# Performance work log

Hardware: AMD Instinct MI355X
Metric: run time of the kernel (lower is better)

The kernel has to match this reference:

```python
import jax, jax.numpy as jnp
import numpy as np

N = 50000   # nodes
E = 640000  # edges
H = 128     # input/hidden dim
C = 40      # classes
L = 2       # gnn layers


def _layernorm(h, g, b, eps=1e-5):
    mu = jnp.mean(h, axis=-1, keepdims=True)
    var = jnp.mean((h - mu) ** 2, axis=-1, keepdims=True)
    return (h - mu) * jax.lax.rsqrt(var + eps) * g + b


def setup_inputs() -> dict:
    key = jax.random.key(0)
    ks = jax.random.split(key, 20)
    s = 0.02
    inp = {
        "x": jax.random.normal(ks[0], (N, H), dtype=jnp.float32),
        "edge_index": jax.random.randint(ks[1], (2, E), 0, N, dtype=jnp.int64),
        # input projection MLP (Linear->ReLU->Dropout(eval)->Linear)
        "proj_w1": jax.random.normal(ks[2], (H, H), dtype=jnp.float32) * s,
        "proj_b1": jnp.zeros((H,), jnp.float32),
        "proj_w2": jax.random.normal(ks[3], (H, H), dtype=jnp.float32) * s,
        "proj_b2": jnp.zeros((H,), jnp.float32),
        "in_norm_g": jnp.ones((H,), jnp.float32),
        "in_norm_b": jnp.zeros((H,), jnp.float32),
        # stacked SAGEConv params: lin_l (on mean-aggregated neighbors, with bias),
        # lin_r (root weight, no bias) -- PyG SAGEConv defaults
        "sage_wl": jax.random.normal(ks[4], (L, H, H), dtype=jnp.float32) * s,
        "sage_bl": jnp.zeros((L, H), jnp.float32),
        "sage_wr": jax.random.normal(ks[5], (L, H, H), dtype=jnp.float32) * s,
        "ln_g": jnp.ones((L, H), jnp.float32),
        "ln_b": jnp.zeros((L, H), jnp.float32),
        # classifier MLP
        "cls_w1": jax.random.normal(ks[6], (H, H), dtype=jnp.float32) * s,
        "cls_b1": jnp.zeros((H,), jnp.float32),
        "cls_w2": jax.random.normal(ks[7], (H, C), dtype=jnp.float32) * s,
        "cls_b2": jnp.zeros((C,), jnp.float32),
    }
    return inp


def reference(x, edge_index, proj_w1, proj_b1, proj_w2, proj_b2,
              in_norm_g, in_norm_b, sage_wl, sage_bl, sage_wr,
              ln_g, ln_b, cls_w1, cls_b1, cls_w2, cls_b2):
    src = edge_index[0]  # message sources x_j
    dst = edge_index[1]  # aggregation targets
    # in-degree counts for mean aggregation (isolated nodes -> 0 output)
    cnt = jax.ops.segment_sum(jnp.ones((E,), jnp.float32), dst, num_segments=N)
    inv_cnt = jnp.where(cnt > 0, 1.0 / jnp.maximum(cnt, 1.0), 0.0)[:, None]

    # input projection + norm (dropout is identity in eval mode)
    h = jax.nn.relu(x @ proj_w1 + proj_b1) @ proj_w2 + proj_b2
    h = _layernorm(h, in_norm_g, in_norm_b)

    for l in range(L):
        msg_sum = jax.ops.segment_sum(h[src], dst, num_segments=N)  # [N,H]
        agg = msg_sum * inv_cnt  # mean aggregation
        h_next = agg @ sage_wl[l] + sage_bl[l] + h @ sage_wr[l]  # SAGEConv
        h_next = jax.nn.relu(h_next)
        h = _layernorm(h + h_next, ln_g[l], ln_b[l])  # residual + LayerNorm

    logits = jax.nn.relu(h @ cls_w1 + cls_b1) @ cls_w2 + cls_b2
    return (logits, h)
```

## Files before the change

### kernel.cpp

```cpp
#include <hip/hip_runtime.h>


namespace {

constexpr int NN = 50000;
constexpr int EE = 640000;
constexpr int HH = 128;
constexpr int CC = 40;
constexpr int SCAN_NB = (NN + 255) / 256;
constexpr int MG = (NN + 127) / 128;
constexpr int DEGB = (EE + 255) / 256;
constexpr int WPB = (5 * 16384 + CC * 128 + 255) / 256;

typedef unsigned short u16;
typedef __attribute__((ext_vector_type(8))) short s16x8;
typedef __attribute__((ext_vector_type(8))) unsigned short u16x8;
typedef __attribute__((ext_vector_type(4))) float f32x4;
typedef __attribute__((ext_vector_type(2))) float f32x2;

__device__ __forceinline__ float b2f(u16 h) {
  unsigned int u = ((unsigned int)h) << 16;
  return __builtin_bit_cast(float, u);
}
__device__ __forceinline__ u16 f2b(float f) {
  unsigned int u = __builtin_bit_cast(unsigned int, f);
  u += 0x7FFFu + ((u >> 16) & 1u);
  return (u16)(u >> 16);
}

__device__ __forceinline__ uint2 pack_fp8(const float* v) {
  int w0 = 0, w1 = 0;
  w0 = __builtin_amdgcn_cvt_pk_fp8_f32(v[0], v[1], w0, false);
  w0 = __builtin_amdgcn_cvt_pk_fp8_f32(v[2], v[3], w0, true);
  w1 = __builtin_amdgcn_cvt_pk_fp8_f32(v[4], v[5], w1, false);
  w1 = __builtin_amdgcn_cvt_pk_fp8_f32(v[6], v[7], w1, true);
  return make_uint2((unsigned)w0, (unsigned)w1);
}
__device__ __forceinline__ void acc_fp8(float* a, uint2 p) {
  const f32x2 f0 = __builtin_amdgcn_cvt_pk_f32_fp8((int)p.x, false);
  const f32x2 f1 = __builtin_amdgcn_cvt_pk_f32_fp8((int)p.x, true);
  const f32x2 f2 = __builtin_amdgcn_cvt_pk_f32_fp8((int)p.y, false);
  const f32x2 f3 = __builtin_amdgcn_cvt_pk_f32_fp8((int)p.y, true);
  a[0] += f0.x; a[1] += f0.y; a[2] += f1.x; a[3] += f1.y;
  a[4] += f2.x; a[5] += f2.y; a[6] += f3.x; a[7] += f3.y;
}

__device__ __forceinline__ s16x8 ldsw(const u16* base, int n, int k0) {
  return *reinterpret_cast<const s16x8*>(base + n * 128 + (((k0 ^ n) & 15) << 3));
}
__device__ __forceinline__ void stsw(u16* base, int r, int c, u16 v) {
  base[r * 128 + ((((c >> 3) ^ r) & 15) << 3) + (c & 7)] = v;
}
template <int NGRAN>
__device__ __forceinline__ void stage(const u16* __restrict__ src, u16* dst, int tid) {
#pragma unroll
  for (int i = 0; i < (NGRAN + 255) / 256; ++i) {
    const int gi = i * 256 + tid;
    if ((NGRAN & 255) == 0 || gi < NGRAN) {
      const int n = gi >> 4, k0 = gi & 15;
      const u16x8 v = *reinterpret_cast<const u16x8*>(src + gi * 8);
      *reinterpret_cast<u16x8*>(dst + n * 128 + (((k0 ^ n) & 15) << 3)) = v;
    }
  }
}

__global__ void k_pre(const float* __restrict__ pw1, const float* __restrict__ pw2,
                      u16* __restrict__ wt, int* __restrict__ cnt) {
  int flat = blockIdx.x * 256 + threadIdx.x;
  const int TWO = 2 * 16384;
  if (flat < TWO) {
    int id = flat >> 14;
    int off = flat & 16383;
    int n = off >> 7, k = off & 127;
    const float* s = id == 0 ? pw1 : pw2;
    wt[(size_t)id * 16384 + n * 128 + k] = f2b(s[k * 128 + n]);
  } else {
    int i = flat - TWO;
    if (i < NN) cnt[i] = 0;
  }
}

__global__ void k_scan_block(const int* __restrict__ cnt, int* __restrict__ rowptr,
                             int* __restrict__ bsum, float* __restrict__ inv) {
  __shared__ int s[256];
  const int t = threadIdx.x;
  const int i = blockIdx.x * 256 + t;
  const int v = i < NN ? cnt[i] : 0;
  s[t] = v;
  __syncthreads();
  for (int off = 1; off < 256; off <<= 1) {
    int add = t >= off ? s[t - off] : 0;
    __syncthreads();
    s[t] += add;
    __syncthreads();
  }
  if (i < NN) {
    rowptr[i] = s[t] - v;
    inv[i] = v > 0 ? 1.0f / (float)v : 0.0f;
  }
  if (t == 255) bsum[blockIdx.x] = s[255];
}

__global__ void k_scan_add(int* __restrict__ rowptr, const int* __restrict__ bsum) {
  __shared__ int s[256];
  const int t = threadIdx.x;
  const int v = t < SCAN_NB ? bsum[t] : 0;
  s[t] = v;
  __syncthreads();
  for (int off = 1; off < 256; off <<= 1) {
    int add = t >= off ? s[t - off] : 0;
    __syncthreads();
    s[t] += add;
    __syncthreads();
  }
  const int boff = blockIdx.x == 0 ? 0 : s[blockIdx.x - 1];
  const int i = blockIdx.x * 256 + t;
  if (i < NN) rowptr[i] += boff;
  if (i == 0) rowptr[NN] = EE;
}

__global__ void k_fill(const int* __restrict__ ei, const int* __restrict__ rowptr,
                       const int* __restrict__ rank, int* __restrict__ col) {
  int e = blockIdx.x * 256 + threadIdx.x;
  if (e >= EE) return;
  const int d = ei[EE + e];
  col[rowptr[d] + rank[e]] = ei[e];
}

__global__ __launch_bounds__(256) void k_gather8(
    const unsigned char* __restrict__ h8, const int* __restrict__ rowptr,
    const int* __restrict__ col, const float* __restrict__ inv,
    u16* __restrict__ agg) {
  const int tid = threadIdx.x;
  const int node = blockIdx.x * 16 + (tid >> 4);
  if (node >= NN) return;
  const int ln = tid & 15;
  const int cl = ln * 8;
  const int start = rowptr[node];
  const int end = rowptr[node + 1];
  float a[8] = {0.f, 0.f, 0.f, 0.f, 0.f, 0.f, 0.f, 0.f};
  int i = start;
  for (; i + 8 <= end; i += 8) {
    const uint2 p0 = *reinterpret_cast<const uint2*>(&h8[(size_t)col[i] * 128 + cl]);
    const uint2 p1 = *reinterpret_cast<const uint2*>(&h8[(size_t)col[i + 1] * 128 + cl]);
    const uint2 p2 = *reinterpret_cast<const uint2*>(&h8[(size_t)col[i + 2] * 128 + cl]);
    const uint2 p3 = *reinterpret_cast<const uint2*>(&h8[(size_t)col[i + 3] * 128 + cl]);
    const uint2 p4 = *reinterpret_cast<const uint2*>(&h8[(size_t)col[i + 4] * 128 + cl]);
    const uint2 p5 = *reinterpret_cast<const uint2*>(&h8[(size_t)col[i + 5] * 128 + cl]);
    const uint2 p6 = *reinterpret_cast<const uint2*>(&h8[(size_t)col[i + 6] * 128 + cl]);
    const uint2 p7 = *reinterpret_cast<const uint2*>(&h8[(size_t)col[i + 7] * 128 + cl]);
    acc_fp8(a, p0); acc_fp8(a, p1); acc_fp8(a, p2); acc_fp8(a, p3);
    acc_fp8(a, p4); acc_fp8(a, p5); acc_fp8(a, p6); acc_fp8(a, p7);
  }
  if (i + 4 <= end) {
    const uint2 p0 = *reinterpret_cast<const uint2*>(&h8[(size_t)col[i] * 128 + cl]);
    const uint2 p1 = *reinterpret_cast<const uint2*>(&h8[(size_t)col[i + 1] * 128 + cl]);
    const uint2 p2 = *reinterpret_cast<const uint2*>(&h8[(size_t)col[i + 2] * 128 + cl]);
    const uint2 p3 = *reinterpret_cast<const uint2*>(&h8[(size_t)col[i + 3] * 128 + cl]);
    acc_fp8(a, p0); acc_fp8(a, p1); acc_fp8(a, p2); acc_fp8(a, p3);
    i += 4;
  }
  for (; i < end; ++i) {
    const uint2 p0 = *reinterpret_cast<const uint2*>(&h8[(size_t)col[i] * 128 + cl]);
    acc_fp8(a, p0);
  }
  const float sc = inv[node];
#pragma unroll
  for (int k = 0; k < 8; ++k)
    agg[(size_t)node * 128 + k * 16 + ln] = f2b(a[k] * sc);
}

__global__ __launch_bounds__(256) void k_mlp_deg(
    const float* __restrict__ x, const u16* __restrict__ WT1,
    const float* __restrict__ pb1, const u16* __restrict__ WT2,
    const float* __restrict__ pb2, const float* __restrict__ lg,
    const float* __restrict__ lb, u16* __restrict__ hb,
    unsigned char* __restrict__ h8,
    const int* __restrict__ ei, int* __restrict__ cnt, int* __restrict__ rank,
    const float* __restrict__ swl, const float* __restrict__ swr,
    const float* __restrict__ cw1, const float* __restrict__ cw2,
    u16* __restrict__ wt) {
  __shared__ u16 lds[32768];
  if (blockIdx.x >= MG) {
    const int rb = blockIdx.x - MG;
    if (rb < DEGB) {
      const int e = rb * 256 + threadIdx.x;
      if (e < EE) rank[e] = atomicAdd(&cnt[ei[EE + e]], 1);
    } else {
      const int flat = (rb - DEGB) * 256 + threadIdx.x;
      const int FIVE = 5 * 16384;
      if (flat < FIVE) {
        int id = flat >> 14;
        int off = flat & 16383;
        int n = off >> 7, k = off & 127;
        const float* s;
        switch (id) {
          case 0: s = swl; break;
          case 1: s = swl + 16384; break;
          case 2: s = swr; break;
          case 3: s = swr + 16384; break;
          default: s = cw1; break;
        }
        wt[(size_t)(id + 2) * 16384 + n * 128 + k] = f2b(s[k * 128 + n]);
      } else {
        int off = flat - FIVE;
        if (off < CC * 128) {
          int n = off >> 7, k = off & 127;
          wt[(size_t)7 * 16384 + n * 128 + k] = f2b(cw2[k * CC + n]);
        }
      }
    }
    return;
  }
  u16* wreg = lds;
  u16* t1r = lds + 16384;
  const int tid = threadIdx.x;
  const int wv = tid >> 6, ln = tid & 63;
  const int lrow = ln & 15, kg = ln >> 4;
  const int tbase = blockIdx.x * 128 + wv * 32;
  const int lb0 = wv * 32;
  const int ar0 = min(tbase + lrow, NN - 1);
  const int ar1 = min(tbase + 16 + lrow, NN - 1);

  stage<2048>(WT1, wreg, tid);
  __syncthreads();

  f32x4 acc0[8], acc1[8];
#pragma unroll
  for (int cf = 0; cf < 8; ++cf) {
    acc0[cf] = (f32x4){0.f, 0.f, 0.f, 0.f};
    acc1[cf] = (f32x4){0.f, 0.f, 0.f, 0.f};
  }
#pragma unroll
  for (int ks = 0; ks < 4; ++ks) {
    const float4* p0 = reinterpret_cast<const float4*>(x + (size_t)ar0 * 128 + ks * 32 + kg * 8);
    const float4* p1 = reinterpret_cast<const float4*>(x + (size_t)ar1 * 128 + ks * 32 + kg * 8);
    float4 x0 = p0[0], x1 = p0[1], y0 = p1[0], y1 = p1[1];
    s16x8 a0, a1;
    a0[0] = (short)f2b(x0.x); a0[1] = (short)f2b(x0.y); a0[2] = (short)f2b(x0.z); a0[3] = (short)f2b(x0.w);
    a0[4] = (short)f2b(x1.x); a0[5] = (short)f2b(x1.y); a0[6] = (short)f2b(x1.z); a0[7] = (short)f2b(x1.w);
    a1[0] = (short)f2b(y0.x); a1[1] = (short)f2b(y0.y); a1[2] = (short)f2b(y0.z); a1[3] = (short)f2b(y0.w);
    a1[4] = (short)f2b(y1.x); a1[5] = (short)f2b(y1.y); a1[6] = (short)f2b(y1.z); a1[7] = (short)f2b(y1.w);
#pragma unroll
    for (int cf = 0; cf < 8; ++cf) {
      const s16x8 bf = ldsw(wreg, cf * 16 + lrow, ks * 4 + kg);
      acc0[cf] = __builtin_amdgcn_mfma_f32_16x16x32_bf16(a0, bf, acc0[cf], 0, 0, 0);
      acc1[cf] = __builtin_amdgcn_mfma_f32_16x16x32_bf16(a1, bf, acc1[cf], 0, 0, 0);
    }
  }
  {
    float bb[8];
#pragma unroll
    for (int cf = 0; cf < 8; ++cf) bb[cf] = pb1[cf * 16 + lrow];
#pragma unroll
    for (int t = 0; t < 2; ++t)
#pragma unroll
      for (int j = 0; j < 4; ++j) {
        const int lr = lb0 + t * 16 + kg * 4 + j;
#pragma unroll
        for (int cf = 0; cf < 8; ++cf)
          stsw(t1r, lr, cf * 16 + lrow, f2b(fmaxf((t ? acc1[cf][j] : acc0[cf][j]) + bb[cf], 0.0f)));
      }
  }
  __syncthreads();
  stage<2048>(WT2, wreg, tid);
  __syncthreads();

  f32x4 c0[8], c1[8];
#pragma unroll
  for (int cf = 0; cf < 8; ++cf) {
    c0[cf] = (f32x4){0.f, 0.f, 0.f, 0.f};
    c1[cf] = (f32x4){0.f, 0.f, 0.f, 0.f};
  }
#pragma unroll
  for (int ks = 0; ks < 4; ++ks) {
    const s16x8 a0 = ldsw(t1r, lb0 + lrow, ks * 4 + kg);
    const s16x8 a1 = ldsw(t1r, lb0 + 16 + lrow, ks * 4 + kg);
#pragma unroll
    for (int cf = 0; cf < 8; ++cf) {
      const s16x8 bf = ldsw(wreg, cf * 16 + lrow, ks * 4 + kg);
      c0[cf] = __builtin_amdgcn_mfma_f32_16x16x32_bf16(a0, bf, c0[cf], 0, 0, 0);
      c1[cf] = __builtin_amdgcn_mfma_f32_16x16x32_bf16(a1, bf, c1[cf], 0, 0, 0);
    }
  }

  float bb[8], gm[8], gb[8];
#pragma unroll
  for (int cf = 0; cf < 8; ++cf) {
    const int c = cf * 16 + lrow;
    bb[cf] = pb2[c];
    gm[cf] = lg[c];
    gb[cf] = lb[c];
  }
#pragma unroll
  for (int t = 0; t < 2; ++t)
#pragma unroll
    for (int j = 0; j < 4; ++j) {
      const int r = tbase + t * 16 + kg * 4 + j;
      float v[8];
#pragma unroll
      for (int cf = 0; cf < 8; ++cf) v[cf] = (t ? c1[cf][j] : c0[cf][j]) + bb[cf];
      float s = 0.f;
#pragma unroll
      for (int cf = 0; cf < 8; ++cf) s += v[cf];
      s += __shfl_xor(s, 1); s += __shfl_xor(s, 2);
      s += __shfl_xor(s, 4); s += __shfl_xor(s, 8);
      const float mu = s * (1.0f / 128);
      float q = 0.f;
#pragma unroll
      for (int cf = 0; cf < 8; ++cf) { const float d = v[cf] - mu; q += d * d; }
      q += __shfl_xor(q, 1); q += __shfl_xor(q, 2);
      q += __shfl_xor(q, 4); q += __shfl_xor(q, 8);
      const float istd = rsqrtf(q * (1.0f / 128) + 1e-5f);
      if (r < NN) {
        float ov[8];
#pragma unroll
        for (int cf = 0; cf < 8; ++cf) {
          ov[cf] = (v[cf] - mu) * istd * gm[cf] + gb[cf];
          hb[(size_t)r * 128 + cf * 16 + lrow] = f2b(ov[cf]);
        }
        *reinterpret_cast<uint2*>(&h8[(size_t)r * 128 + lrow * 8]) = pack_fp8(ov);
      }
    }
}

__global__ __launch_bounds__(256) void k_sage0(
    const u16* __restrict__ agg, const u16* __restrict__ hb,
    const u16* __restrict__ WTl, const u16* __restrict__ WTr,
    const float* __restrict__ bl, const float* __restrict__ lg,
    const float* __restrict__ lb, u16* __restrict__ hb_out,
    unsigned char* __restrict__ h8) {
  __shared__ u16 lds[32768];
  u16* wl = lds;
  u16* wr = lds + 16384;
  const int tid = threadIdx.x;
  const int wv = tid >> 6, ln = tid & 63;
  const int lrow = ln & 15, kg = ln >> 4;
  const int tbase = blockIdx.x * 128 + wv * 32;
  const int ar0 = min(tbase + lrow, NN - 1);
  const int ar1 = min(tbase + 16 + lrow, NN - 1);

  stage<2048>(WTl, wl, tid);
  stage<2048>(WTr, wr, tid);
  __syncthreads();

  f32x4 acc0[8], acc1[8];
#pragma unroll
  for (int cf = 0; cf < 8; ++cf) {
    acc0[cf] = (f32x4){0.f, 0.f, 0.f, 0.f};
    acc1[cf] = (f32x4){0.f, 0.f, 0.f, 0.f};
  }
#pragma unroll
  for (int ks = 0; ks < 4; ++ks) {
    const s16x8 g0 = *reinterpret_cast<const s16x8*>(agg + (size_t)ar0 * 128 + ks * 32 + kg * 8);
    const s16x8 g1 = *reinterpret_cast<const s16x8*>(agg + (size_t)ar1 * 128 + ks * 32 + kg * 8);
    const s16x8 h0 = *reinterpret_cast<const s16x8*>(hb + (size_t)ar0 * 128 + ks * 32 + kg * 8);
    const s16x8 h1 = *reinterpret_cast<const s16x8*>(hb + (size_t)ar1 * 128 + ks * 32 + kg * 8);
#pragma unroll
    for (int cf = 0; cf < 8; ++cf) {
      const s16x8 bwl = ldsw(wl, cf * 16 + lrow, ks * 4 + kg);
      const s16x8 bwr = ldsw(wr, cf * 16 + lrow, ks * 4 + kg);
      acc0[cf] = __builtin_amdgcn_mfma_f32_16x16x32_bf16(g0, bwl, acc0[cf], 0, 0, 0);
      acc0[cf] = __builtin_amdgcn_mfma_f32_16x16x32_bf16(h0, bwr, acc0[cf], 0, 0, 0);
      acc1[cf] = __builtin_amdgcn_mfma_f32_16x16x32_bf16(g1, bwl, acc1[cf], 0, 0, 0);
      acc1[cf] = __builtin_amdgcn_mfma_f32_16x16x32_bf16(h1, bwr, acc1[cf], 0, 0, 0);
    }
  }

  float bb[8], gm[8], gb[8];
#pragma unroll
  for (int cf = 0; cf < 8; ++cf) {
    const int c = cf * 16 + lrow;
    bb[cf] = bl[c];
    gm[cf] = lg[c];
    gb[cf] = lb[c];
  }
#pragma unroll
  for (int t = 0; t < 2; ++t)
#pragma unroll
    for (int j = 0; j < 4; ++j) {
      const int r = tbase + t * 16 + kg * 4 + j;
      const int rs = r < NN ? r : NN - 1;
      float v[8];
#pragma unroll
      for (int cf = 0; cf < 8; ++cf) {
        const int c = cf * 16 + lrow;
        v[cf] = b2f(hb[(size_t)rs * 128 + c]) +
                fmaxf((t ? acc1[cf][j] : acc0[cf][j]) + bb[cf], 0.0f);
      }
      float s = 0.f;
#pragma unroll
      for (int cf = 0; cf < 8; ++cf) s += v[cf];
      s += __shfl_xor(s, 1); s += __shfl_xor(s, 2);
      s += __shfl_xor(s, 4); s += __shfl_xor(s, 8);
      const float mu = s * (1.0f / 128);
      float q = 0.f;
#pragma unroll
      for (int cf = 0; cf < 8; ++cf) { const float d = v[cf] - mu; q += d * d; }
      q += __shfl_xor(q, 1); q += __shfl_xor(q, 2);
      q += __shfl_xor(q, 4); q += __shfl_xor(q, 8);
      const float istd = rsqrtf(q * (1.0f / 128) + 1e-5f);
      if (r < NN) {
        float ov[8];
#pragma unroll
        for (int cf = 0; cf < 8; ++cf) {
          ov[cf] = (v[cf] - mu) * istd * gm[cf] + gb[cf];
          hb_out[(size_t)r * 128 + cf * 16 + lrow] = f2b(ov[cf]);
        }
        *reinterpret_cast<uint2*>(&h8[(size_t)r * 128 + lrow * 8]) = pack_fp8(ov);
      }
    }
}

__global__ __launch_bounds__(256) void k_sage_cls(
    const u16* __restrict__ agg, const u16* __restrict__ hb,
    const u16* __restrict__ WTl, const u16* __restrict__ WTr,
    const float* __restrict__ bl, const float* __restrict__ lg,
    const float* __restrict__ lb,
    const u16* __restrict__ Wc1, const float* __restrict__ cb1,
    const u16* __restrict__ Wc2, const float* __restrict__ cb2,
    float* __restrict__ out_h, float* __restrict__ logits) {
  __shared__ u16 lds[37888];
  u16* wl = lds;
  u16* wr = lds + 16384;
  u16* w2 = lds + 32768;
  const int tid = threadIdx.x;
  const int wv = tid >> 6, ln = tid & 63;
  const int lrow = ln & 15, kg = ln >> 4;
  const int tbase = blockIdx.x * 128 + wv * 32;
  const int lb0 = wv * 32;
  const int ar0 = min(tbase + lrow, NN - 1);
  const int ar1 = min(tbase + 16 + lrow, NN - 1);

  stage<2048>(WTl, wl, tid);
  stage<2048>(WTr, wr, tid);
  stage<640>(Wc2, w2, tid);
  __syncthreads();

  f32x4 acc0[8], acc1[8];
#pragma unroll
  for (int cf = 0; cf < 8; ++cf) {
    acc0[cf] = (f32x4){0.f, 0.f, 0.f, 0.f};
    acc1[cf] = (f32x4){0.f, 0.f, 0.f, 0.f};
  }
#pragma unroll
  for (int ks = 0; ks < 4; ++ks) {
    const s16x8 g0 = *reinterpret_cast<const s16x8*>(agg + (size_t)ar0 * 128 + ks * 32 + kg * 8);
    const s16x8 g1 = *reinterpret_cast<const s16x8*>(agg + (size_t)ar1 * 128 + ks * 32 + kg * 8);
    const s16x8 h0 = *reinterpret_cast<const s16x8*>(hb + (size_t)ar0 * 128 + ks * 32 + kg * 8);
    const s16x8 h1 = *reinterpret_cast<const s16x8*>(hb + (size_t)ar1 * 128 + ks * 32 + kg * 8);
#pragma unroll
    for (int cf = 0; cf < 8; ++cf) {
      const s16x8 bwl = ldsw(wl, cf * 16 + lrow, ks * 4 + kg);
      const s16x8 bwr = ldsw(wr, cf * 16 + lrow, ks * 4 + kg);
      acc0[cf] = __builtin_amdgcn_mfma_f32_16x16x32_bf16(g0, bwl, acc0[cf], 0, 0, 0);
      acc0[cf] = __builtin_amdgcn_mfma_f32_16x16x32_bf16(h0, bwr, acc0[cf], 0, 0, 0);
      acc1[cf] = __builtin_amdgcn_mfma_f32_16x16x32_bf16(g1, bwl, acc1[cf], 0, 0, 0);
      acc1[cf] = __builtin_amdgcn_mfma_f32_16x16x32_bf16(h1, bwr, acc1[cf], 0, 0, 0);
    }
  }
  __syncthreads();

  {
    float bb[8], gm[8], gb[8];
#pragma unroll
    for (int cf = 0; cf < 8; ++cf) {
      const int c = cf * 16 + lrow;
      bb[cf] = bl[c];
      gm[cf] = lg[c];
      gb[cf] = lb[c];
    }
#pragma unroll
    for (int t = 0; t < 2; ++t)
#pragma unroll
      for (int j = 0; j < 4; ++j) {
        const int r = tbase + t * 16 + kg * 4 + j;
        const int rs = r < NN ? r : NN - 1;
        const int lr = lb0 + t * 16 + kg * 4 + j;
        float v[8];
#pragma unroll
        for (int cf = 0; cf < 8; ++cf) {
          const int c = cf * 16 + lrow;
          v[cf] = b2f(hb[(size_t)rs * 128 + c]) +
                  fmaxf((t ? acc1[cf][j] : acc0[cf][j]) + bb[cf], 0.0f);
        }
        float s = 0.f;
#pragma unroll
        for (int cf = 0; cf < 8; ++cf) s += v[cf];
        s += __shfl_xor(s, 1); s += __shfl_xor(s, 2);
        s += __shfl_xor(s, 4); s += __shfl_xor(s, 8);
        const float mu = s * (1.0f / 128);
        float q = 0.f;
#pragma unroll
        for (int cf = 0; cf < 8; ++cf) { const float d = v[cf] - mu; q += d * d; }
        q += __shfl_xor(q, 1); q += __shfl_xor(q, 2);
        q += __shfl_xor(q, 4); q += __shfl_xor(q, 8);
        const float istd = rsqrtf(q * (1.0f / 128) + 1e-5f);
#pragma unroll
        for (int cf = 0; cf < 8; ++cf) {
          const int c = cf * 16 + lrow;
          const float o = (v[cf] - mu) * istd * gm[cf] + gb[cf];
          stsw(wl, lr, c, f2b(o));
          if (r < NN) out_h[(size_t)r * 128 + c] = o;
        }
      }
  }
  stage<2048>(Wc1, wr, tid);
  __syncthreads();

  float cb1v[8];
#pragma unroll
  for (int cf = 0; cf < 8; ++cf) cb1v[cf] = cb1[cf * 16 + lrow];

#pragma unroll
  for (int t = 0; t < 2; ++t) {
    const int rb = lb0 + t * 16;
    f32x4 a3[8];
#pragma unroll
    for (int cf = 0; cf < 8; ++cf) a3[cf] = (f32x4){0.f, 0.f, 0.f, 0.f};
#pragma unroll
    for (int ks = 0; ks < 4; ++ks) {
      const s16x8 a = ldsw(wl, rb + lrow, ks * 4 + kg);
#pragma unroll
      for (int cf = 0; cf < 8; ++cf) {
        const s16x8 bf = ldsw(wr, cf * 16 + lrow, ks * 4 + kg);
        a3[cf] = __builtin_amdgcn_mfma_f32_16x16x32_bf16(a, bf, a3[cf], 0, 0, 0);
      }
    }
#pragma unroll
    for (int j = 0; j < 4; ++j)
#pragma unroll
      for (int cf = 0; cf < 8; ++cf)
        stsw(wl, rb + kg * 4 + j, cf * 16 + lrow, f2b(fmaxf(a3[cf][j] + cb1v[cf], 0.0f)));

    f32x4 a2[3];
#pragma unroll
    for (int cf = 0; cf < 3; ++cf) a2[cf] = (f32x4){0.f, 0.f, 0.f, 0.f};
#pragma unroll
    for (int ks = 0; ks < 4; ++ks) {
      const s16x8 a = ldsw(wl, rb + lrow, ks * 4 + kg);
#pragma unroll
      for (int cf = 0; cf < 3; ++cf) {
        const int bn = min(cf * 16 + lrow, CC - 1);
        const s16x8 bf = ldsw(w2, bn, ks * 4 + kg);
        a2[cf] = __builtin_amdgcn_mfma_f32_16x16x32_bf16(a, bf, a2[cf], 0, 0, 0);
      }
    }
#pragma unroll
    for (int j = 0; j < 4; ++j) {
      const int r = tbase + t * 16 + kg * 4 + j;
      if (r < NN) {
#pragma unroll
        for (int cf = 0; cf < 3; ++cf) {
          const int c = cf * 16 + lrow;
          if (c < CC) logits[(size_t)r * CC + c] = a2[cf][j] + cb2[c];
        }
      }
    }
  }
}

}

extern "C" void kernel_launch(void* const* d_in, const int* in_sizes, int n_in,
                              void* d_out, int out_size, void* d_ws, size_t ws_size,
                              hipStream_t stream) {
  (void)in_sizes; (void)n_in; (void)out_size; (void)ws_size;
  const float* x   = (const float*)d_in[0];
  const int*   ei  = (const int*)d_in[1];
  const float* pw1 = (const float*)d_in[2];
  const float* pb1 = (const float*)d_in[3];
  const float* pw2 = (const float*)d_in[4];
  const float* pb2 = (const float*)d_in[5];
  const float* ing = (const float*)d_in[6];
  const float* inb = (const float*)d_in[7];
  const float* swl = (const float*)d_in[8];
  const float* sbl = (const float*)d_in[9];
  const float* swr = (const float*)d_in[10];
  const float* lng = (const float*)d_in[11];
  const float* lnb = (const float*)d_in[12];
  const float* cw1 = (const float*)d_in[13];
  const float* cb1 = (const float*)d_in[14];
  const float* cw2 = (const float*)d_in[15];
  const float* cb2 = (const float*)d_in[16];

  float* out_logits = (float*)d_out;
  float* out_h = out_logits + (size_t)NN * CC;

  const size_t NNH = (size_t)NN * HH;
  u16*   hb   = (u16*)d_ws;
  u16*   bufA = hb + NNH;
  u16*   wt   = bufA + NNH;
  int*   cnt    = (int*)(wt + 8 * 16384);
  float* inv    = (float*)(cnt + NN);
  int*   rowptr = (int*)(inv + NN);
  int*   bsum   = rowptr + NN + 1;
  int*   colarr = bsum + 256;
  int*   rankar = colarr + EE;
  unsigned char* h8 = (unsigned char*)(rankar + EE);

  const int PRE_B = (2 * 16384 + NN + 255) / 256;
  k_pre<<<PRE_B, 256, 0, stream>>>(pw1, pw2, wt, cnt);

  k_mlp_deg<<<MG + DEGB + WPB, 256, 0, stream>>>(
      x, wt + 0 * 16384, pb1, wt + 1 * 16384, pb2, ing, inb, hb, h8,
      ei, cnt, rankar, swl, swr, cw1, cw2, wt);

  k_scan_block<<<SCAN_NB, 256, 0, stream>>>(cnt, rowptr, bsum, inv);
  k_scan_add<<<SCAN_NB, 256, 0, stream>>>(rowptr, bsum);
  k_fill<<<(EE + 255) / 256, 256, 0, stream>>>(ei, rowptr, rankar, colarr);

  k_gather8<<<(NN + 15) / 16, 256, 0, stream>>>(h8, rowptr, colarr, inv, bufA);
  k_sage0<<<(NN + 127) / 128, 256, 0, stream>>>(
      bufA, hb, wt + 2 * 16384, wt + 4 * 16384, sbl, lng, lnb, hb, h8);

  k_gather8<<<(NN + 15) / 16, 256, 0, stream>>>(h8, rowptr, colarr, inv, bufA);
  k_sage_cls<<<(NN + 127) / 128, 256, 0, stream>>>(
      bufA, hb, wt + 3 * 16384, wt + 5 * 16384, sbl + HH, lng + HH, lnb + HH,
      wt + 6 * 16384, cb1, wt + 7 * 16384, cb2, out_h, out_logits);
}
```

Measured before the change: 142.9 us.

## Fuse CSR column fill into input MLP kernel and move degree counting earlier

Reshuffles the preprocessing schedule. Degree counting with atomics and all weight transposes now run in one early kernel after a separate zeroing kernel. The CSR column fill is merged with the input MLP so its scatter overlaps with the MLP compute instead of running as a standalone kernel after the scan. This keeps the launch count the same but moves the atomic degree pass off the MLP kernel. The scan now sits between degree counting and the MLP, so the MLP can no longer overlap with the atomics.

```diff
diff --git a/kernel.cpp b/kernel.cpp
--- a/kernel.cpp
+++ b/kernel.cpp
@@ -9,8 +9,8 @@
 constexpr int CC = 40;
 constexpr int SCAN_NB = (NN + 255) / 256;
 constexpr int MG = (NN + 127) / 128;
-constexpr int DEGB = (EE + 255) / 256;
-constexpr int WPB = (5 * 16384 + CC * 128 + 255) / 256;
+constexpr int FILLB = (EE + 255) / 256;
+constexpr int WTB = (7 * 16384 + CC * 128 + 255) / 256;
 
 typedef unsigned short u16;
 typedef __attribute__((ext_vector_type(8))) short s16x8;
@@ -64,19 +64,45 @@
   }
 }
 
-__global__ void k_pre(const float* __restrict__ pw1, const float* __restrict__ pw2,
-                      u16* __restrict__ wt, int* __restrict__ cnt) {
+__global__ void k_zero(int* __restrict__ p) {
+  const int i = blockIdx.x * 256 + threadIdx.x;
+  if (i < NN) p[i] = 0;
+}
+
+__global__ void k_pre_deg(const float* __restrict__ pw1, const float* __restrict__ pw2,
+                          const float* __restrict__ swl, const float* __restrict__ swr,
+                          const float* __restrict__ cw1, const float* __restrict__ cw2,
+                          u16* __restrict__ wt,
+                          const int* __restrict__ ei, int* __restrict__ cnt,
+                          int* __restrict__ rank) {
+  if (blockIdx.x >= WTB) {
+    const int e = (blockIdx.x - WTB) * 256 + threadIdx.x;
+    if (e < EE) rank[e] = atomicAdd(&cnt[ei[EE + e]], 1);
+    return;
+  }
   int flat = blockIdx.x * 256 + threadIdx.x;
-  const int TWO = 2 * 16384;
-  if (flat < TWO) {
+  const int SEVEN = 7 * 16384;
+  if (flat < SEVEN) {
     int id = flat >> 14;
     int off = flat & 16383;
     int n = off >> 7, k = off & 127;
-    const float* s = id == 0 ? pw1 : pw2;
+    const float* s;
+    switch (id) {
+      case 0: s = pw1; break;
+      case 1: s = pw2; break;
+      case 2: s = swl; break;
+      case 3: s = swl + 16384; break;
+      case 4: s = swr; break;
+      case 5: s = swr + 16384; break;
+      default: s = cw1; break;
+    }
     wt[(size_t)id * 16384 + n * 128 + k] = f2b(s[k * 128 + n]);
   } else {
-    int i = flat - TWO;
-    if (i < NN) cnt[i] = 0;
+    int off = flat - SEVEN;
+    if (off < CC * 128) {
+      int n = off >> 7, k = off & 127;
+      wt[(size_t)7 * 16384 + n * 128 + k] = f2b(cw2[k * CC + n]);
+    }
   }
 }
 
@@ -117,14 +143,6 @@
   const int i = blockIdx.x * 256 + t;
   if (i < NN) rowptr[i] += boff;
   if (i == 0) rowptr[NN] = EE;
-}
-
-__global__ void k_fill(const int* __restrict__ ei, const int* __restrict__ rowptr,
-                       const int* __restrict__ rank, int* __restrict__ col) {
-  int e = blockIdx.x * 256 + threadIdx.x;
-  if (e >= EE) return;
-  const int d = ei[EE + e];
-  col[rowptr[d] + rank[e]] = ei[e];
 }
 
 __global__ __launch_bounds__(256) void k_gather8(
@@ -170,45 +188,20 @@
     agg[(size_t)node * 128 + k * 16 + ln] = f2b(a[k] * sc);
 }
 
-__global__ __launch_bounds__(256) void k_mlp_deg(
+__global__ __launch_bounds__(256) void k_fill_mlp(
     const float* __restrict__ x, const u16* __restrict__ WT1,
     const float* __restrict__ pb1, const u16* __restrict__ WT2,
     const float* __restrict__ pb2, const float* __restrict__ lg,
     const float* __restrict__ lb, u16* __restrict__ hb,
     unsigned char* __restrict__ h8,
-    const int* __restrict__ ei, int* __restrict__ cnt, int* __restrict__ rank,
-    const float* __restrict__ swl, const float* __restrict__ swr,
-    const float* __restrict__ cw1, const float* __restrict__ cw2,
-    u16* __restrict__ wt) {
+    const int* __restrict__ ei, const int* __restrict__ rowptr,
+    const int* __restrict__ rank, int* __restrict__ col) {
   __shared__ u16 lds[32768];
   if (blockIdx.x >= MG) {
-    const int rb = blockIdx.x - MG;
-    if (rb < DEGB) {
-      const int e = rb * 256 + threadIdx.x;
-      if (e < EE) rank[e] = atomicAdd(&cnt[ei[EE + e]], 1);
-    } else {
-      const int flat = (rb - DEGB) * 256 + threadIdx.x;
-      const int FIVE = 5 * 16384;
-      if (flat < FIVE) {
-        int id = flat >> 14;
-        int off = flat & 16383;
-        int n = off >> 7, k = off & 127;
-        const float* s;
-        switch (id) {
-          case 0: s = swl; break;
-          case 1: s = swl + 16384; break;
-          case 2: s = swr; break;
-          case 3: s = swr + 16384; break;
-          default: s = cw1; break;
-        }
-        wt[(size_t)(id + 2) * 16384 + n * 128 + k] = f2b(s[k * 128 + n]);
-      } else {
-        int off = flat - FIVE;
-        if (off < CC * 128) {
-          int n = off >> 7, k = off & 127;
-          wt[(size_t)7 * 16384 + n * 128 + k] = f2b(cw2[k * CC + n]);
-        }
-      }
+    const int e = (blockIdx.x - MG) * 256 + threadIdx.x;
+    if (e < EE) {
+      const int d = ei[EE + e];
+      col[rowptr[d] + rank[e]] = ei[e];
     }
     return;
   }
@@ -599,16 +592,16 @@
   int*   rankar = colarr + EE;
   unsigned char* h8 = (unsigned char*)(rankar + EE);
 
-  const int PRE_B = (2 * 16384 + NN + 255) / 256;
-  k_pre<<<PRE_B, 256, 0, stream>>>(pw1, pw2, wt, cnt);
-
-  k_mlp_deg<<<MG + DEGB + WPB, 256, 0, stream>>>(
-      x, wt + 0 * 16384, pb1, wt + 1 * 16384, pb2, ing, inb, hb, h8,
-      ei, cnt, rankar, swl, swr, cw1, cw2, wt);
+  k_zero<<<SCAN_NB, 256, 0, stream>>>(cnt);
+  k_pre_deg<<<WTB + FILLB, 256, 0, stream>>>(
+      pw1, pw2, swl, swr, cw1, cw2, wt, ei, cnt, rankar);
 
   k_scan_block<<<SCAN_NB, 256, 0, stream>>>(cnt, rowptr, bsum, inv);
   k_scan_add<<<SCAN_NB, 256, 0, stream>>>(rowptr, bsum);
-  k_fill<<<(EE + 255) / 256, 256, 0, stream>>>(ei, rowptr, rankar, colarr);
+
+  k_fill_mlp<<<MG + FILLB, 256, 0, stream>>>(
+      x, wt + 0 * 16384, pb1, wt + 1 * 16384, pb2, ing, inb, hb, h8,
+      ei, rowptr, rankar, colarr);
 
   k_gather8<<<(NN + 15) / 16, 256, 0, stream>>>(h8, rowptr, colarr, inv, bufA);
   k_sage0<<<(NN + 127) / 128, 256, 0, stream>>>(
```

Measured after the change: 149.4 us. +4.6%, slower.

## Fuse scan-add with CSR fill and store column indices as 16-bit

Applied to the files above, without the earlier changes.

Merges the block-offset scan-add kernel with the CSR column-fill kernel. Each block redundantly scans the block sums and then either writes the final row pointers or scatters edges using the local offset plus the block offset, which removes one launch and the dependency between the two steps. Column indices are stored as u16, halving index traffic in the gather kernels. N=50000 fits in 16 bits, but the narrower index type ties the code to graphs under 65536 nodes.

```diff
diff --git a/kernel.cpp b/kernel.cpp
--- a/kernel.cpp
+++ b/kernel.cpp
@@ -11,6 +11,7 @@
 constexpr int MG = (NN + 127) / 128;
 constexpr int DEGB = (EE + 255) / 256;
 constexpr int WPB = (5 * 16384 + CC * 128 + 255) / 256;
+constexpr int FILLB = (EE + 255) / 256;
 
 typedef unsigned short u16;
 typedef __attribute__((ext_vector_type(8))) short s16x8;
@@ -80,7 +81,7 @@
   }
 }
 
-__global__ void k_scan_block(const int* __restrict__ cnt, int* __restrict__ rowptr,
+__global__ void k_scan_block(const int* __restrict__ cnt, int* __restrict__ rloc,
                              int* __restrict__ bsum, float* __restrict__ inv) {
   __shared__ int s[256];
   const int t = threadIdx.x;
@@ -95,41 +96,48 @@
     __syncthreads();
   }
   if (i < NN) {
-    rowptr[i] = s[t] - v;
+    rloc[i] = s[t] - v;
     inv[i] = v > 0 ? 1.0f / (float)v : 0.0f;
   }
   if (t == 255) bsum[blockIdx.x] = s[255];
 }
 
-__global__ void k_scan_add(int* __restrict__ rowptr, const int* __restrict__ bsum) {
+__global__ void k_scanfill(const int* __restrict__ rloc, const int* __restrict__ bsum,
+                           int* __restrict__ rpf,
+                           const int* __restrict__ ei, const int* __restrict__ rank,
+                           u16* __restrict__ col) {
   __shared__ int s[256];
   const int t = threadIdx.x;
-  const int v = t < SCAN_NB ? bsum[t] : 0;
-  s[t] = v;
-  __syncthreads();
-  for (int off = 1; off < 256; off <<= 1) {
-    int add = t >= off ? s[t - off] : 0;
+  {
+    const int v = t < SCAN_NB ? bsum[t] : 0;
+    s[t] = v;
     __syncthreads();
-    s[t] += add;
-    __syncthreads();
-  }
-  const int boff = blockIdx.x == 0 ? 0 : s[blockIdx.x - 1];
-  const int i = blockIdx.x * 256 + t;
-  if (i < NN) rowptr[i] += boff;
-  if (i == 0) rowptr[NN] = EE;
-}
-
-__global__ void k_fill(const int* __restrict__ ei, const int* __restrict__ rowptr,
-                       const int* __restrict__ rank, int* __restrict__ col) {
-  int e = blockIdx.x * 256 + threadIdx.x;
-  if (e >= EE) return;
-  const int d = ei[EE + e];
-  col[rowptr[d] + rank[e]] = ei[e];
+    for (int off = 1; off < 256; off <<= 1) {
+      int add = t >= off ? s[t - off] : 0;
+      __syncthreads();
+      s[t] += add;
+      __syncthreads();
+    }
+  }
+  if (blockIdx.x < SCAN_NB) {
+    const int boff = blockIdx.x == 0 ? 0 : s[blockIdx.x - 1];
+    const int i = blockIdx.x * 256 + t;
+    if (i < NN) rpf[i] = rloc[i] + boff;
+    if (i == 0) rpf[NN] = EE;
+  } else {
+    const int e = (blockIdx.x - SCAN_NB) * 256 + t;
+    if (e < EE) {
+      const int d = ei[EE + e];
+      const int bd = d >> 8;
+      const int boff = bd == 0 ? 0 : s[bd - 1];
+      col[rloc[d] + boff + rank[e]] = (u16)ei[e];
+    }
+  }
 }
 
 __global__ __launch_bounds__(256) void k_gather8(
     const unsigned char* __restrict__ h8, const int* __restrict__ rowptr,
-    const int* __restrict__ col, const float* __restrict__ inv,
+    const u16* __restrict__ col, const float* __restrict__ inv,
     u16* __restrict__ agg) {
   const int tid = threadIdx.x;
   const int node = blockIdx.x * 16 + (tid >> 4);
@@ -141,22 +149,25 @@
   float a[8] = {0.f, 0.f, 0.f, 0.f, 0.f, 0.f, 0.f, 0.f};
   int i = start;
   for (; i + 8 <= end; i += 8) {
-    const uint2 p0 = *reinterpret_cast<const uint2*>(&h8[(size_t)col[i] * 128 + cl]);
-    const uint2 p1 = *reinterpret_cast<const uint2*>(&h8[(size_t)col[i + 1] * 128 + cl]);
-    const uint2 p2 = *reinterpret_cast<const uint2*>(&h8[(size_t)col[i + 2] * 128 + cl]);
-    const uint2 p3 = *reinterpret_cast<const uint2*>(&h8[(size_t)col[i + 3] * 128 + cl]);
-    const uint2 p4 = *reinterpret_cast<const uint2*>(&h8[(size_t)col[i + 4] * 128 + cl]);
-    const uint2 p5 = *reinterpret_cast<const uint2*>(&h8[(size_t)col[i + 5] * 128 + cl]);
-    const uint2 p6 = *reinterpret_cast<const uint2*>(&h8[(size_t)col[i + 6] * 128 + cl]);
-    const uint2 p7 = *reinterpret_cast<const uint2*>(&h8[(size_t)col[i + 7] * 128 + cl]);
+    const int s0 = col[i], s1 = col[i + 1], s2 = col[i + 2], s3 = col[i + 3];
+    const int s4 = col[i + 4], s5 = col[i + 5], s6 = col[i + 6], s7 = col[i + 7];
+    const uint2 p0 = *reinterpret_cast<const uint2*>(&h8[(size_t)s0 * 128 + cl]);
+    const uint2 p1 = *reinterpret_cast<const uint2*>(&h8[(size_t)s1 * 128 + cl]);
+    const uint2 p2 = *reinterpret_cast<const uint2*>(&h8[(size_t)s2 * 128 + cl]);
+    const uint2 p3 = *reinterpret_cast<const uint2*>(&h8[(size_t)s3 * 128 + cl]);
+    const uint2 p4 = *reinterpret_cast<const uint2*>(&h8[(size_t)s4 * 128 + cl]);
+    const uint2 p5 = *reinterpret_cast<const uint2*>(&h8[(size_t)s5 * 128 + cl]);
+    const uint2 p6 = *reinterpret_cast<const uint2*>(&h8[(size_t)s6 * 128 + cl]);
+    const uint2 p7 = *reinterpret_cast<const uint2*>(&h8[(size_t)s7 * 128 + cl]);
     acc_fp8(a, p0); acc_fp8(a, p1); acc_fp8(a, p2); acc_fp8(a, p3);
     acc_fp8(a, p4); acc_fp8(a, p5); acc_fp8(a, p6); acc_fp8(a, p7);
   }
   if (i + 4 <= end) {
-    const uint2 p0 = *reinterpret_cast<const uint2*>(&h8[(size_t)col[i] * 128 + cl]);
-    const uint2 p1 = *reinterpret_cast<const uint2*>(&h8[(size_t)col[i + 1] * 128 + cl]);
-    const uint2 p2 = *reinterpret_cast<const uint2*>(&h8[(size_t)col[i + 2] * 128 + cl]);
-    const uint2 p3 = *reinterpret_cast<const uint2*>(&h8[(size_t)col[i + 3] * 128 + cl]);
+    const int s0 = col[i], s1 = col[i + 1], s2 = col[i + 2], s3 = col[i + 3];
+    const uint2 p0 = *reinterpret_cast<const uint2*>(&h8[(size_t)s0 * 128 + cl]);
+    const uint2 p1 = *reinterpret_cast<const uint2*>(&h8[(size_t)s1 * 128 + cl]);
+    const uint2 p2 = *reinterpret_cast<const uint2*>(&h8[(size_t)s2 * 128 + cl]);
+    const uint2 p3 = *reinterpret_cast<const uint2*>(&h8[(size_t)s3 * 128 + cl]);
     acc_fp8(a, p0); acc_fp8(a, p1); acc_fp8(a, p2); acc_fp8(a, p3);
     i += 4;
   }
@@ -593,11 +604,12 @@
   u16*   wt   = bufA + NNH;
   int*   cnt    = (int*)(wt + 8 * 16384);
   float* inv    = (float*)(cnt + NN);
-  int*   rowptr = (int*)(inv + NN);
-  int*   bsum   = rowptr + NN + 1;
-  int*   colarr = bsum + 256;
-  int*   rankar = colarr + EE;
-  unsigned char* h8 = (unsigned char*)(rankar + EE);
+  int*   rloc   = (int*)(inv + NN);
+  int*   rpf    = rloc + NN;
+  int*   bsum   = rpf + NN + 1;
+  int*   rankar = bsum + 256;
+  u16*   colarr = (u16*)(rankar + EE);
+  unsigned char* h8 = (unsigned char*)(colarr + EE);
 
   const int PRE_B = (2 * 16384 + NN + 255) / 256;
   k_pre<<<PRE_B, 256, 0, stream>>>(pw1, pw2, wt, cnt);
@@ -606,15 +618,14 @@
       x, wt + 0 * 16384, pb1, wt + 1 * 16384, pb2, ing, inb, hb, h8,
       ei, cnt, rankar, swl, swr, cw1, cw2, wt);
 
-  k_scan_block<<<SCAN_NB, 256, 0, stream>>>(cnt, rowptr, bsum, inv);
-  k_scan_add<<<SCAN_NB, 256, 0, stream>>>(rowptr, bsum);
-  k_fill<<<(EE + 255) / 256, 256, 0, stream>>>(ei, rowptr, rankar, colarr);
-
-  k_gather8<<<(NN + 15) / 16, 256, 0, stream>>>(h8, rowptr, colarr, inv, bufA);
+  k_scan_block<<<SCAN_NB, 256, 0, stream>>>(cnt, rloc, bsum, inv);
+  k_scanfill<<<SCAN_NB + FILLB, 256, 0, stream>>>(rloc, bsum, rpf, ei, rankar, colarr);
+
+  k_gather8<<<(NN + 15) / 16, 256, 0, stream>>>(h8, rpf, colarr, inv, bufA);
   k_sage0<<<(NN + 127) / 128, 256, 0, stream>>>(
       bufA, hb, wt + 2 * 16384, wt + 4 * 16384, sbl, lng, lnb, hb, h8);
 
-  k_gather8<<<(NN + 15) / 16, 256, 0, stream>>>(h8, rowptr, colarr, inv, bufA);
+  k_gather8<<<(NN + 15) / 16, 256, 0, stream>>>(h8, rpf, colarr, inv, bufA);
   k_sage_cls<<<(NN + 127) / 128, 256, 0, stream>>>(
       bufA, hb, wt + 3 * 16384, wt + 5 * 16384, sbl + HH, lng + HH, lnb + HH,
       wt + 6 * 16384, cb1, wt + 7 * 16384, cb2, out_h, out_logits);
```

Result: no change. 140.1 us, median of 2 (-1.9%).
